# Kernel tuning notes

Measured on AMD Instinct MI355X. Metric: run time of the kernel, lower is better.

Reference implementation:

```python
import jax, jax.numpy as jnp
import numpy as np
from jax import lax

B, T, S = 8, 4096, 64  # batch, time steps, hidden states


def setup_inputs() -> dict:
    key = jax.random.key(0)
    k1, k2 = jax.random.split(key)
    # log-domain pairwise factors: log_factors[b, t, i, j] = log p(z_{t+1}=j, x_t | z_t=i)
    log_factors = jax.random.normal(k1, (B, T, S, S), dtype=jnp.float32)
    # initial log factor over the first state
    log_init = jax.random.normal(k2, (B, S), dtype=jnp.float32)
    return {"log_factors": log_factors, "log_init": log_init}


def reference(log_factors, log_init):
    """HMM forward algorithm: sequential logaddexp/add chain reduction over time.

    Equivalent to sequential_sum_product(logaddexp, add, log_factors, 'time')
    followed by adding log_init over 'state' and reducing all with logaddexp.
    Implemented as the O(T*S^2) alpha-recursion (vector carry) rather than the
    O(T*S^3) matrix chain -- same math, efficient form.
    """
    fs = jnp.moveaxis(log_factors, 1, 0)  # [T, B, S, S]

    def step(alpha, f_t):
        # alpha: [B, S] over state i ; f_t: [B, S, S] over (i, j)
        alpha_next = jax.nn.logsumexp(alpha[:, :, None] + f_t, axis=1)  # [B, S]
        return alpha_next, None

    alpha_T, _ = lax.scan(step, log_init, fs)
    return jax.nn.logsumexp(alpha_T, axis=-1)  # [B] log-normalizer
```

## Files before the change

### kernel.cpp

```cpp
#include <hip/hip_runtime.h>


#define HMM_B 8
#define HMM_T 4096
#define HMM_S 64
#define HMM_C 128
#define HMM_L (HMM_T / HMM_C)

typedef __attribute__((ext_vector_type(8))) short s16x8;
typedef __attribute__((ext_vector_type(4))) float f32x4;
typedef __attribute__((ext_vector_type(4))) unsigned int u32x4;

__device__ inline void gld16(const float* g, const float* l) {
  __builtin_amdgcn_global_load_lds((const __attribute__((address_space(1))) void*)g,
                                   (__attribute__((address_space(3))) void*)l, 16, 0, 0);
}

__device__ inline unsigned cvtpk(float lo, float hi) {
  unsigned r;
  asm("v_cvt_pk_bf16_f32 %0, %1, %2" : "=v"(r) : "v"(lo), "v"(hi));
  return r;
}

__device__ inline float dpp_fmax16(float x) {
  int xi = __float_as_int(x);
  x = fmaxf(x, __int_as_float(__builtin_amdgcn_mov_dpp(xi, 0xB1, 0xF, 0xF, 1)));
  xi = __float_as_int(x);
  x = fmaxf(x, __int_as_float(__builtin_amdgcn_mov_dpp(xi, 0x4E, 0xF, 0xF, 1)));
  xi = __float_as_int(x);
  x = fmaxf(x, __int_as_float(__builtin_amdgcn_mov_dpp(xi, 0x141, 0xF, 0xF, 1)));
  xi = __float_as_int(x);
  x = fmaxf(x, __int_as_float(__builtin_amdgcn_mov_dpp(xi, 0x140, 0xF, 0xF, 1)));
  return x;
}

__device__ inline float bflo(unsigned w) { return __uint_as_float(w << 16); }
__device__ inline float bfhi(unsigned w) { return __uint_as_float(w & 0xffff0000u); }


__global__ __launch_bounds__(256, 3)
void hmm_phase1(const float* __restrict__ lf, unsigned short* __restrict__ wsE,
                unsigned short* __restrict__ wsEt, float* __restrict__ wsM) {
  __shared__ struct {
    float fbuf[2][4096];
    unsigned short fB[4096];
    unsigned short escr[4][1408];
  } sm;

  const int tid = threadIdx.x;
  const int w   = tid >> 6;
  const int l   = tid & 63;
  const int wg  = blockIdx.x;
  const int bb  = wg >> 7;
  const int cc  = wg & (HMM_C - 1);
  const float* fbase = lf + ((size_t)(bb * HMM_T + cc * HMM_L)) * (HMM_S * HMM_S);

  auto issue = [&](int t) {
    const int par = t & 1;
    const float* fb = fbase + (size_t)t * 4096;
#pragma unroll
    for (int u = 0; u < 4; ++u) {
      int slot = (w * 4 + u) * 64 + l;
      int k    = slot >> 4;
      int q16  = slot & 15;
      const float* src = fb + k * 64 + ((q16 ^ (k & 7)) << 2);
      gld16(src, &sm.fbuf[par][(w * 4 + u) * 256]);
    }
  };

  issue(0);

  float mracc0 = 0.f, mracc1 = 0.f, mracc2 = 0.f, mracc3 = 0.f;
  const int c4 = l & 15, q = l >> 4;

  for (int t = 0; t < HMM_L; ++t) {
    const int par = t & 1;
    if (t + 1 < HMM_L) issue(t + 1);

    if (t < HMM_L - 1) asm volatile("s_waitcnt vmcnt(4)" ::: "memory");
    else               asm volatile("s_waitcnt vmcnt(0)" ::: "memory");
    __builtin_amdgcn_sched_barrier(0);

#pragma unroll
    for (int u = 0; u < 2; ++u) {
      const int g = 2 * w + (l >> 5);
      const int j = (l & 31) + 32 * u;
      float v[8];
#pragma unroll
      for (int e = 0; e < 8; ++e) {
        int k = 8 * g + e;
        v[e] = sm.fbuf[par][k * 64 + (((j >> 2) ^ (k & 7)) << 2) + (j & 3)];
      }
      unsigned p0 = cvtpk(__expf(v[0]), __expf(v[1]));
      unsigned p1 = cvtpk(__expf(v[2]), __expf(v[3]));
      unsigned p2 = cvtpk(__expf(v[4]), __expf(v[5]));
      unsigned p3 = cvtpk(__expf(v[6]), __expf(v[7]));
      int slot = ((g >> 2) * 4 + (j >> 4)) * 64 + ((g & 3) << 4) + (j & 15);
      u32x4 o; o.x = p0; o.y = p1; o.z = p2; o.w = p3;
      *(u32x4*)&sm.fB[slot * 8] = o;
    }

    asm volatile("s_waitcnt lgkmcnt(0)" ::: "memory");
    __builtin_amdgcn_sched_barrier(0);
    __builtin_amdgcn_s_barrier();

    s16x8 a0, a1;
    if (t == 0) {
      const int iloc = 16 * w + (l & 15);
      const int kb0 = (l >> 4) * 8, kb1 = 32 + (l >> 4) * 8;
#pragma unroll
      for (int e = 0; e < 8; ++e) {
        a0[e] = (short)((kb0 + e == iloc) ? 0x3F80 : 0);
        a1[e] = (short)((kb1 + e == iloc) ? 0x3F80 : 0);
      }
    } else {
      a0 = *(const s16x8*)&sm.escr[w][(l & 15) * 88 + ((l >> 4) * 8)];
      a1 = *(const s16x8*)&sm.escr[w][(l & 15) * 88 + 32 + ((l >> 4) * 8)];
    }

    f32x4 acc[4];
#pragma unroll
    for (int n = 0; n < 4; ++n) {
      s16x8 b0 = *(const s16x8*)&sm.fB[((0 + n) * 64 + l) * 8];
      s16x8 b1 = *(const s16x8*)&sm.fB[((4 + n) * 64 + l) * 8];
      f32x4 c = {0.f, 0.f, 0.f, 0.f};
      c = __builtin_amdgcn_mfma_f32_16x16x32_bf16(a0, b0, c, 0, 0, 0);
      c = __builtin_amdgcn_mfma_f32_16x16x32_bf16(a1, b1, c, 0, 0, 0);
      acc[n] = c;
    }

    float inv[4];
    {
      float m0 = fmaxf(fmaxf(acc[0][0], acc[1][0]), fmaxf(acc[2][0], acc[3][0]));
      float m1 = fmaxf(fmaxf(acc[0][1], acc[1][1]), fmaxf(acc[2][1], acc[3][1]));
      float m2 = fmaxf(fmaxf(acc[0][2], acc[1][2]), fmaxf(acc[2][2], acc[3][2]));
      float m3 = fmaxf(fmaxf(acc[0][3], acc[1][3]), fmaxf(acc[2][3], acc[3][3]));
      m0 = dpp_fmax16(m0); m1 = dpp_fmax16(m1);
      m2 = dpp_fmax16(m2); m3 = dpp_fmax16(m3);
      mracc0 += __log2f(m0); mracc1 += __log2f(m1);
      mracc2 += __log2f(m2); mracc3 += __log2f(m3);
      inv[0] = __builtin_amdgcn_rcpf(m0); inv[1] = __builtin_amdgcn_rcpf(m1);
      inv[2] = __builtin_amdgcn_rcpf(m2); inv[3] = __builtin_amdgcn_rcpf(m3);
    }
#pragma unroll
    for (int n = 0; n < 4; ++n) {
      unsigned p0 = cvtpk(acc[n][0] * inv[0], acc[n][1] * inv[1]);
      unsigned p1 = cvtpk(acc[n][2] * inv[2], acc[n][3] * inv[3]);
      sm.escr[w][(4 * q + 0) * 88 + 16 * n + c4] = (unsigned short)(p0 & 0xffffu);
      sm.escr[w][(4 * q + 1) * 88 + 16 * n + c4] = (unsigned short)(p0 >> 16);
      sm.escr[w][(4 * q + 2) * 88 + 16 * n + c4] = (unsigned short)(p1 & 0xffffu);
      sm.escr[w][(4 * q + 3) * 88 + 16 * n + c4] = (unsigned short)(p1 >> 16);
    }
    __syncthreads();
  }

  {
    const size_t cb = ((size_t)(bb * HMM_C + cc)) * 4096;
    const int j = tid & 63, p4 = tid >> 6;
    unsigned short o0[8], o1[8];
#pragma unroll
    for (int rl = 0; rl < 8; ++rl)  o0[rl] = sm.escr[p4][rl * 88 + j];
#pragma unroll
    for (int rl = 0; rl < 8; ++rl)  o1[rl] = sm.escr[p4][(rl + 8) * 88 + j];
    *(u32x4*)&wsEt[cb + j * 64 + p4 * 16]     = *(u32x4*)o0;
    *(u32x4*)&wsEt[cb + j * 64 + p4 * 16 + 8] = *(u32x4*)o1;

    const int r = tid >> 2, jq = tid & 3;
    u32x4 v0 = *(const u32x4*)&sm.escr[r >> 4][(r & 15) * 88 + jq * 16];
    u32x4 v1 = *(const u32x4*)&sm.escr[r >> 4][(r & 15) * 88 + jq * 16 + 8];
    *(u32x4*)&wsE[cb + r * 64 + jq * 16]     = v0;
    *(u32x4*)&wsE[cb + r * 64 + jq * 16 + 8] = v1;

    if (c4 == 0) {
      const float ln2 = 0.6931471805599453f;
      float* dst = wsM + (size_t)(bb * HMM_C + cc) * 64 + 16 * w + 4 * q;
      dst[0] = mracc0 * ln2; dst[1] = mracc1 * ln2;
      dst[2] = mracc2 * ln2; dst[3] = mracc3 * ln2;
    }
  }
}


__global__ __launch_bounds__(64)
void hmm_combine(const unsigned short* __restrict__ inE,
                 const unsigned short* __restrict__ inEt,
                 const float* __restrict__ inM, int inBS,
                 unsigned short* __restrict__ outE,
                 unsigned short* __restrict__ outEt,
                 float* __restrict__ outM, int outBS, int nOut) {
  __shared__ float sS[64];
  __shared__ float sM1[64];
  const int l = threadIdx.x, c4 = l & 15, q = l >> 4;
  const int b = blockIdx.x / nOut, p = blockIdx.x % nOut;
  const size_t li = (size_t)(b * inBS + 2 * p) * 4096;
  const size_t ri = li + 4096;
  const float* m1p = inM + (size_t)(b * inBS + 2 * p) * 64;

  float m2v = m1p[64 + l];
  float m1v = m1p[l];
  float mu = m2v;
  mu = fmaxf(mu, __shfl_xor(mu, 1));  mu = fmaxf(mu, __shfl_xor(mu, 2));
  mu = fmaxf(mu, __shfl_xor(mu, 4));  mu = fmaxf(mu, __shfl_xor(mu, 8));
  mu = fmaxf(mu, __shfl_xor(mu, 16)); mu = fmaxf(mu, __shfl_xor(mu, 32));
  sS[l] = __expf(m2v - mu);
  sM1[l] = m1v;
  __syncthreads();

  const unsigned short* E1 = inE + li;
  s16x8 afr[4][2];
#pragma unroll
  for (int m = 0; m < 4; ++m)
#pragma unroll
    for (int h = 0; h < 2; ++h)
      afr[m][h] = *(const s16x8*)&E1[(m * 16 + c4) * 64 + h * 32 + q * 8];

  const unsigned short* Et2 = inEt + ri;
  s16x8 bfr[2][4];
#pragma unroll
  for (int h = 0; h < 2; ++h) {
    f32x4 s0 = *(const f32x4*)&sS[h * 32 + q * 8];
    f32x4 s1 = *(const f32x4*)&sS[h * 32 + q * 8 + 4];
#pragma unroll
    for (int n = 0; n < 4; ++n) {
      u32x4 raw = *(const u32x4*)&Et2[(n * 16 + c4) * 64 + h * 32 + q * 8];
      unsigned p0 = cvtpk(bflo(raw.x) * s0[0], bfhi(raw.x) * s0[1]);
      unsigned p1 = cvtpk(bflo(raw.y) * s0[2], bfhi(raw.y) * s0[3]);
      unsigned p2 = cvtpk(bflo(raw.z) * s1[0], bfhi(raw.z) * s1[1]);
      unsigned p3 = cvtpk(bflo(raw.w) * s1[2], bfhi(raw.w) * s1[3]);
      u32x4 o; o.x = p0; o.y = p1; o.z = p2; o.w = p3;
      bfr[h][n] = *(s16x8*)&o;
    }
  }

  f32x4 acc[4][4];
#pragma unroll
  for (int m = 0; m < 4; ++m)
#pragma unroll
    for (int n = 0; n < 4; ++n) {
      f32x4 c = {0.f, 0.f, 0.f, 0.f};
      c = __builtin_amdgcn_mfma_f32_16x16x32_bf16(afr[m][0], bfr[0][n], c, 0, 0, 0);
      c = __builtin_amdgcn_mfma_f32_16x16x32_bf16(afr[m][1], bfr[1][n], c, 0, 0, 0);
      acc[m][n] = c;
    }

  const size_t oi = (size_t)(b * outBS + p) * 4096;
  unsigned short* Eo  = outE + oi;
  unsigned short* Eto = outEt + oi;
  float* mo = outM + (size_t)(b * outBS + p) * 64;

#pragma unroll
  for (int m = 0; m < 4; ++m) {
    float rmax[4];
#pragma unroll
    for (int r = 0; r < 4; ++r) {
      float v = fmaxf(fmaxf(acc[m][0][r], acc[m][1][r]),
                      fmaxf(acc[m][2][r], acc[m][3][r]));
      v = fmaxf(v, __shfl_xor(v, 1));
      v = fmaxf(v, __shfl_xor(v, 2));
      v = fmaxf(v, __shfl_xor(v, 4));
      v = fmaxf(v, __shfl_xor(v, 8));
      rmax[r] = v;
    }
    float inv[4] = {__builtin_amdgcn_rcpf(rmax[0]), __builtin_amdgcn_rcpf(rmax[1]),
                    __builtin_amdgcn_rcpf(rmax[2]), __builtin_amdgcn_rcpf(rmax[3])};
#pragma unroll
    for (int n = 0; n < 4; ++n) {
      unsigned p01 = cvtpk(acc[m][n][0] * inv[0], acc[m][n][1] * inv[1]);
      unsigned p23 = cvtpk(acc[m][n][2] * inv[2], acc[m][n][3] * inv[3]);
      unsigned long long packed = (unsigned long long)p01 |
                                  ((unsigned long long)p23 << 32);
      *(unsigned long long*)&Eto[(16 * n + c4) * 64 + 16 * m + 4 * q] = packed;
      Eo[(16 * m + 4 * q + 0) * 64 + 16 * n + c4] = (unsigned short)(p01 & 0xffffu);
      Eo[(16 * m + 4 * q + 1) * 64 + 16 * n + c4] = (unsigned short)(p01 >> 16);
      Eo[(16 * m + 4 * q + 2) * 64 + 16 * n + c4] = (unsigned short)(p23 & 0xffffu);
      Eo[(16 * m + 4 * q + 3) * 64 + 16 * n + c4] = (unsigned short)(p23 >> 16);
    }
    if (c4 == 0) {
#pragma unroll
      for (int r = 0; r < 4; ++r) {
        int i = 16 * m + 4 * q + r;
        mo[i] = sM1[i] + mu + __logf(rmax[r]);
      }
    }
  }
}


__global__ __launch_bounds__(64)
void hmm_final(const unsigned short* __restrict__ E, const float* __restrict__ M,
               int bs, const float* __restrict__ linit, float* __restrict__ out) {
  const int b = blockIdx.x, l = threadIdx.x;
  const unsigned short* Eb = E + (size_t)b * bs * 4096;
  float av = linit[b * 64 + l] + M[(size_t)b * bs * 64 + l];
  float mx = av;
  mx = fmaxf(mx, __shfl_xor(mx, 1));  mx = fmaxf(mx, __shfl_xor(mx, 2));
  mx = fmaxf(mx, __shfl_xor(mx, 4));  mx = fmaxf(mx, __shfl_xor(mx, 8));
  mx = fmaxf(mx, __shfl_xor(mx, 16)); mx = fmaxf(mx, __shfl_xor(mx, 32));
  float u = __expf(av - mx);
  float rs = 0.f;
#pragma unroll
  for (int e = 0; e < 8; ++e) {
    u32x4 raw = *(const u32x4*)&Eb[l * 64 + e * 8];
    rs += bflo(raw.x) + bfhi(raw.x) + bflo(raw.y) + bfhi(raw.y) +
          bflo(raw.z) + bfhi(raw.z) + bflo(raw.w) + bfhi(raw.w);
  }
  float s = u * rs;
  s += __shfl_xor(s, 1);  s += __shfl_xor(s, 2);  s += __shfl_xor(s, 4);
  s += __shfl_xor(s, 8);  s += __shfl_xor(s, 16); s += __shfl_xor(s, 32);
  if (l == 0) out[b] = mx + __logf(s);
}

extern "C" void kernel_launch(void* const* d_in, const int* in_sizes, int n_in,
                              void* d_out, int out_size, void* d_ws, size_t ws_size,
                              hipStream_t stream) {
  (void)in_sizes; (void)n_in; (void)out_size; (void)ws_size;
  const float* lf    = (const float*)d_in[0];
  const float* linit = (const float*)d_in[1];
  float* out = (float*)d_out;

  unsigned short* E_A  = (unsigned short*)d_ws;
  unsigned short* Et_A = E_A + (size_t)1024 * 4096;
  float*          M_A  = (float*)(Et_A + (size_t)1024 * 4096);
  unsigned short* E_B  = (unsigned short*)(M_A + (size_t)1024 * 64);
  unsigned short* Et_B = E_B + (size_t)512 * 4096;
  float*          M_B  = (float*)(Et_B + (size_t)512 * 4096);

  hmm_phase1<<<dim3(HMM_B * HMM_C), dim3(256), 0, stream>>>(lf, E_A, Et_A, M_A);

  hmm_combine<<<dim3(8 * 64), dim3(64), 0, stream>>>(E_A, Et_A, M_A, 128,
                                                     E_B, Et_B, M_B, 64, 64);
  hmm_combine<<<dim3(8 * 32), dim3(64), 0, stream>>>(E_B, Et_B, M_B, 64,
                                                     E_A, Et_A, M_A, 128, 32);
  hmm_combine<<<dim3(8 * 16), dim3(64), 0, stream>>>(E_A, Et_A, M_A, 128,
                                                     E_B, Et_B, M_B, 64, 16);
  hmm_combine<<<dim3(8 * 8),  dim3(64), 0, stream>>>(E_B, Et_B, M_B, 64,
                                                     E_A, Et_A, M_A, 128, 8);
  hmm_combine<<<dim3(8 * 4),  dim3(64), 0, stream>>>(E_A, Et_A, M_A, 128,
                                                     E_B, Et_B, M_B, 64, 4);
  hmm_combine<<<dim3(8 * 2),  dim3(64), 0, stream>>>(E_B, Et_B, M_B, 64,
                                                     E_A, Et_A, M_A, 128, 2);
  hmm_combine<<<dim3(8 * 1),  dim3(64), 0, stream>>>(E_A, Et_A, M_A, 128,
                                                     E_B, Et_B, M_B, 64, 1);

  hmm_final<<<dim3(HMM_B), dim3(64), 0, stream>>>(E_B, M_B, 64, linit, out);
}
```

Baseline: 208.2 us.

## Replace tree of combine launches with sequential 16-chunk combine and vector final pass

Result: slower. 229.2 us (+10.1%).

```diff
diff --git a/kernel.cpp b/kernel.cpp
--- a/kernel.cpp
+++ b/kernel.cpp
@@ -69,13 +69,13 @@
   };
 
   issue(0);
+  issue(1);
 
   float mracc0 = 0.f, mracc1 = 0.f, mracc2 = 0.f, mracc3 = 0.f;
   const int c4 = l & 15, q = l >> 4;
 
   for (int t = 0; t < HMM_L; ++t) {
     const int par = t & 1;
-    if (t + 1 < HMM_L) issue(t + 1);
 
     if (t < HMM_L - 1) asm volatile("s_waitcnt vmcnt(4)" ::: "memory");
     else               asm volatile("s_waitcnt vmcnt(0)" ::: "memory");
@@ -103,6 +103,9 @@
     asm volatile("s_waitcnt lgkmcnt(0)" ::: "memory");
     __builtin_amdgcn_sched_barrier(0);
     __builtin_amdgcn_s_barrier();
+    __builtin_amdgcn_sched_barrier(0);
+
+    if (t + 2 < HMM_L) issue(t + 2);
 
     s16x8 a0, a1;
     if (t == 0) {
@@ -151,8 +154,14 @@
       sm.escr[w][(4 * q + 2) * 88 + 16 * n + c4] = (unsigned short)(p1 & 0xffffu);
       sm.escr[w][(4 * q + 3) * 88 + 16 * n + c4] = (unsigned short)(p1 >> 16);
     }
-    __syncthreads();
-  }
+
+    asm volatile("s_waitcnt lgkmcnt(0)" ::: "memory");
+    __builtin_amdgcn_sched_barrier(0);
+    __builtin_amdgcn_s_barrier();
+    __builtin_amdgcn_sched_barrier(0);
+  }
+
+  __syncthreads();
 
   {
     const size_t cb = ((size_t)(bb * HMM_C + cc)) * 4096;
@@ -165,11 +174,13 @@
     *(u32x4*)&wsEt[cb + j * 64 + p4 * 16]     = *(u32x4*)o0;
     *(u32x4*)&wsEt[cb + j * 64 + p4 * 16 + 8] = *(u32x4*)o1;
 
-    const int r = tid >> 2, jq = tid & 3;
-    u32x4 v0 = *(const u32x4*)&sm.escr[r >> 4][(r & 15) * 88 + jq * 16];
-    u32x4 v1 = *(const u32x4*)&sm.escr[r >> 4][(r & 15) * 88 + jq * 16 + 8];
-    *(u32x4*)&wsE[cb + r * 64 + jq * 16]     = v0;
-    *(u32x4*)&wsE[cb + r * 64 + jq * 16 + 8] = v1;
+    if ((cc & 15) == 0) {
+      const int r = tid >> 2, jq = tid & 3;
+      u32x4 v0 = *(const u32x4*)&sm.escr[r >> 4][(r & 15) * 88 + jq * 16];
+      u32x4 v1 = *(const u32x4*)&sm.escr[r >> 4][(r & 15) * 88 + jq * 16 + 8];
+      *(u32x4*)&wsE[cb + r * 64 + jq * 16]     = v0;
+      *(u32x4*)&wsE[cb + r * 64 + jq * 16 + 8] = v1;
+    }
 
     if (c4 == 0) {
       const float ln2 = 0.6931471805599453f;
@@ -182,129 +193,215 @@
 
 
 __global__ __launch_bounds__(64)
-void hmm_combine(const unsigned short* __restrict__ inE,
-                 const unsigned short* __restrict__ inEt,
-                 const float* __restrict__ inM, int inBS,
-                 unsigned short* __restrict__ outE,
-                 unsigned short* __restrict__ outEt,
-                 float* __restrict__ outM, int outBS, int nOut) {
+void hmm_combine16(const unsigned short* __restrict__ inE,
+                   const unsigned short* __restrict__ inEt,
+                   const float* __restrict__ inM,
+                   unsigned short* __restrict__ outEt,
+                   float* __restrict__ outM) {
   __shared__ float sS[64];
-  __shared__ float sM1[64];
+  __shared__ float sM[64];
+  __shared__ unsigned short pL[4096];
+
   const int l = threadIdx.x, c4 = l & 15, q = l >> 4;
-  const int b = blockIdx.x / nOut, p = blockIdx.x % nOut;
-  const size_t li = (size_t)(b * inBS + 2 * p) * 4096;
-  const size_t ri = li + 4096;
-  const float* m1p = inM + (size_t)(b * inBS + 2 * p) * 64;
-
-  float m2v = m1p[64 + l];
-  float m1v = m1p[l];
-  float mu = m2v;
-  mu = fmaxf(mu, __shfl_xor(mu, 1));  mu = fmaxf(mu, __shfl_xor(mu, 2));
-  mu = fmaxf(mu, __shfl_xor(mu, 4));  mu = fmaxf(mu, __shfl_xor(mu, 8));
-  mu = fmaxf(mu, __shfl_xor(mu, 16)); mu = fmaxf(mu, __shfl_xor(mu, 32));
-  sS[l] = __expf(m2v - mu);
-  sM1[l] = m1v;
-  __syncthreads();
-
-  const unsigned short* E1 = inE + li;
+  const int b = blockIdx.x >> 3, g = blockIdx.x & 7;
+  const int cbase = b * HMM_C + g * 16;
+
   s16x8 afr[4][2];
 #pragma unroll
   for (int m = 0; m < 4; ++m)
 #pragma unroll
     for (int h = 0; h < 2; ++h)
-      afr[m][h] = *(const s16x8*)&E1[(m * 16 + c4) * 64 + h * 32 + q * 8];
-
-  const unsigned short* Et2 = inEt + ri;
-  s16x8 bfr[2][4];
-#pragma unroll
-  for (int h = 0; h < 2; ++h) {
-    f32x4 s0 = *(const f32x4*)&sS[h * 32 + q * 8];
-    f32x4 s1 = *(const f32x4*)&sS[h * 32 + q * 8 + 4];
-#pragma unroll
-    for (int n = 0; n < 4; ++n) {
-      u32x4 raw = *(const u32x4*)&Et2[(n * 16 + c4) * 64 + h * 32 + q * 8];
-      unsigned p0 = cvtpk(bflo(raw.x) * s0[0], bfhi(raw.x) * s0[1]);
-      unsigned p1 = cvtpk(bflo(raw.y) * s0[2], bfhi(raw.y) * s0[3]);
-      unsigned p2 = cvtpk(bflo(raw.z) * s1[0], bfhi(raw.z) * s1[1]);
-      unsigned p3 = cvtpk(bflo(raw.w) * s1[2], bfhi(raw.w) * s1[3]);
-      u32x4 o; o.x = p0; o.y = p1; o.z = p2; o.w = p3;
-      bfr[h][n] = *(s16x8*)&o;
-    }
-  }
-
-  f32x4 acc[4][4];
-#pragma unroll
-  for (int m = 0; m < 4; ++m)
-#pragma unroll
-    for (int n = 0; n < 4; ++n) {
-      f32x4 c = {0.f, 0.f, 0.f, 0.f};
-      c = __builtin_amdgcn_mfma_f32_16x16x32_bf16(afr[m][0], bfr[0][n], c, 0, 0, 0);
-      c = __builtin_amdgcn_mfma_f32_16x16x32_bf16(afr[m][1], bfr[1][n], c, 0, 0, 0);
-      acc[m][n] = c;
-    }
-
-  const size_t oi = (size_t)(b * outBS + p) * 4096;
-  unsigned short* Eo  = outE + oi;
-  unsigned short* Eto = outEt + oi;
-  float* mo = outM + (size_t)(b * outBS + p) * 64;
-
-#pragma unroll
-  for (int m = 0; m < 4; ++m) {
-    float rmax[4];
-#pragma unroll
-    for (int r = 0; r < 4; ++r) {
-      float v = fmaxf(fmaxf(acc[m][0][r], acc[m][1][r]),
-                      fmaxf(acc[m][2][r], acc[m][3][r]));
-      v = fmaxf(v, __shfl_xor(v, 1));
-      v = fmaxf(v, __shfl_xor(v, 2));
-      v = fmaxf(v, __shfl_xor(v, 4));
-      v = fmaxf(v, __shfl_xor(v, 8));
-      rmax[r] = v;
-    }
-    float inv[4] = {__builtin_amdgcn_rcpf(rmax[0]), __builtin_amdgcn_rcpf(rmax[1]),
-                    __builtin_amdgcn_rcpf(rmax[2]), __builtin_amdgcn_rcpf(rmax[3])};
-#pragma unroll
-    for (int n = 0; n < 4; ++n) {
-      unsigned p01 = cvtpk(acc[m][n][0] * inv[0], acc[m][n][1] * inv[1]);
-      unsigned p23 = cvtpk(acc[m][n][2] * inv[2], acc[m][n][3] * inv[3]);
-      unsigned long long packed = (unsigned long long)p01 |
-                                  ((unsigned long long)p23 << 32);
-      *(unsigned long long*)&Eto[(16 * n + c4) * 64 + 16 * m + 4 * q] = packed;
-      Eo[(16 * m + 4 * q + 0) * 64 + 16 * n + c4] = (unsigned short)(p01 & 0xffffu);
-      Eo[(16 * m + 4 * q + 1) * 64 + 16 * n + c4] = (unsigned short)(p01 >> 16);
-      Eo[(16 * m + 4 * q + 2) * 64 + 16 * n + c4] = (unsigned short)(p23 & 0xffffu);
-      Eo[(16 * m + 4 * q + 3) * 64 + 16 * n + c4] = (unsigned short)(p23 >> 16);
-    }
+      afr[m][h] = *(const s16x8*)&inE[(size_t)cbase * 4096 +
+                                      (m * 16 + c4) * 64 + h * 32 + q * 8];
+  sM[l] = inM[(size_t)cbase * 64 + l];
+
+  u32x4 braw[2][4];
+  float mv;
+  {
+    const unsigned short* Et = inEt + (size_t)(cbase + 1) * 4096;
+#pragma unroll
+    for (int h = 0; h < 2; ++h)
+#pragma unroll
+      for (int n = 0; n < 4; ++n)
+        braw[h][n] = *(const u32x4*)&Et[(n * 16 + c4) * 64 + h * 32 + q * 8];
+    mv = inM[(size_t)(cbase + 1) * 64 + l];
+  }
+
+  for (int c = 1; c < 16; ++c) {
+    u32x4 bcur[2][4];
+#pragma unroll
+    for (int h = 0; h < 2; ++h)
+#pragma unroll
+      for (int n = 0; n < 4; ++n) bcur[h][n] = braw[h][n];
+    float mcur = mv;
+    if (c < 15) {
+      const unsigned short* Et = inEt + (size_t)(cbase + c + 1) * 4096;
+#pragma unroll
+      for (int h = 0; h < 2; ++h)
+#pragma unroll
+        for (int n = 0; n < 4; ++n)
+          braw[h][n] = *(const u32x4*)&Et[(n * 16 + c4) * 64 + h * 32 + q * 8];
+      mv = inM[(size_t)(cbase + c + 1) * 64 + l];
+    }
+
+    float nu = mcur;
+    nu = fmaxf(nu, __shfl_xor(nu, 1));  nu = fmaxf(nu, __shfl_xor(nu, 2));
+    nu = fmaxf(nu, __shfl_xor(nu, 4));  nu = fmaxf(nu, __shfl_xor(nu, 8));
+    nu = fmaxf(nu, __shfl_xor(nu, 16)); nu = fmaxf(nu, __shfl_xor(nu, 32));
+    sS[l] = __expf(mcur - nu);
+
+    s16x8 bfr[2][4];
+#pragma unroll
+    for (int h = 0; h < 2; ++h) {
+      f32x4 s0 = *(const f32x4*)&sS[h * 32 + q * 8];
+      f32x4 s1 = *(const f32x4*)&sS[h * 32 + q * 8 + 4];
+#pragma unroll
+      for (int n = 0; n < 4; ++n) {
+        u32x4 raw = bcur[h][n];
+        unsigned p0 = cvtpk(bflo(raw.x) * s0[0], bfhi(raw.x) * s0[1]);
+        unsigned p1 = cvtpk(bflo(raw.y) * s0[2], bfhi(raw.y) * s0[3]);
+        unsigned p2 = cvtpk(bflo(raw.z) * s1[0], bfhi(raw.z) * s1[1]);
+        unsigned p3 = cvtpk(bflo(raw.w) * s1[2], bfhi(raw.w) * s1[3]);
+        u32x4 o; o.x = p0; o.y = p1; o.z = p2; o.w = p3;
+        bfr[h][n] = *(s16x8*)&o;
+      }
+    }
+
+    f32x4 acc[4][4];
+#pragma unroll
+    for (int m = 0; m < 4; ++m)
+#pragma unroll
+      for (int n = 0; n < 4; ++n) {
+        f32x4 cc2 = {0.f, 0.f, 0.f, 0.f};
+        cc2 = __builtin_amdgcn_mfma_f32_16x16x32_bf16(afr[m][0], bfr[0][n], cc2, 0, 0, 0);
+        cc2 = __builtin_amdgcn_mfma_f32_16x16x32_bf16(afr[m][1], bfr[1][n], cc2, 0, 0, 0);
+        acc[m][n] = cc2;
+      }
+
+    float rmax[4][4];
+#pragma unroll
+    for (int m = 0; m < 4; ++m)
+#pragma unroll
+      for (int r = 0; r < 4; ++r) {
+        float v = fmaxf(fmaxf(acc[m][0][r], acc[m][1][r]),
+                        fmaxf(acc[m][2][r], acc[m][3][r]));
+        v = fmaxf(v, __shfl_xor(v, 1));
+        v = fmaxf(v, __shfl_xor(v, 2));
+        v = fmaxf(v, __shfl_xor(v, 4));
+        v = fmaxf(v, __shfl_xor(v, 8));
+        rmax[m][r] = v;
+      }
     if (c4 == 0) {
 #pragma unroll
-      for (int r = 0; r < 4; ++r) {
-        int i = 16 * m + 4 * q + r;
-        mo[i] = sM1[i] + mu + __logf(rmax[r]);
-      }
-    }
-  }
-}
-
+      for (int m = 0; m < 4; ++m)
+#pragma unroll
+        for (int r = 0; r < 4; ++r)
+          sM[16 * m + 4 * q + r] += nu + __logf(rmax[m][r]);
+    }
+
+    if (c < 15) {
+#pragma unroll
+      for (int m = 0; m < 4; ++m) {
+        float i0 = __builtin_amdgcn_rcpf(rmax[m][0]);
+        float i1 = __builtin_amdgcn_rcpf(rmax[m][1]);
+        float i2 = __builtin_amdgcn_rcpf(rmax[m][2]);
+        float i3 = __builtin_amdgcn_rcpf(rmax[m][3]);
+#pragma unroll
+        for (int n = 0; n < 4; ++n) {
+          unsigned p01 = cvtpk(acc[m][n][0] * i0, acc[m][n][1] * i1);
+          unsigned p23 = cvtpk(acc[m][n][2] * i2, acc[m][n][3] * i3);
+          pL[(16 * m + 4 * q + 0) * 64 + 16 * n + c4] = (unsigned short)(p01 & 0xffffu);
+          pL[(16 * m + 4 * q + 1) * 64 + 16 * n + c4] = (unsigned short)(p01 >> 16);
+          pL[(16 * m + 4 * q + 2) * 64 + 16 * n + c4] = (unsigned short)(p23 & 0xffffu);
+          pL[(16 * m + 4 * q + 3) * 64 + 16 * n + c4] = (unsigned short)(p23 >> 16);
+        }
+      }
+#pragma unroll
+      for (int m = 0; m < 4; ++m)
+#pragma unroll
+        for (int h = 0; h < 2; ++h)
+          afr[m][h] = *(const s16x8*)&pL[(m * 16 + c4) * 64 + h * 32 + q * 8];
+    } else {
+      const size_t oi = (size_t)(b * 8 + g) * 4096;
+#pragma unroll
+      for (int m = 0; m < 4; ++m) {
+        float i0 = __builtin_amdgcn_rcpf(rmax[m][0]);
+        float i1 = __builtin_amdgcn_rcpf(rmax[m][1]);
+        float i2 = __builtin_amdgcn_rcpf(rmax[m][2]);
+        float i3 = __builtin_amdgcn_rcpf(rmax[m][3]);
+#pragma unroll
+        for (int n = 0; n < 4; ++n) {
+          unsigned p01 = cvtpk(acc[m][n][0] * i0, acc[m][n][1] * i1);
+          unsigned p23 = cvtpk(acc[m][n][2] * i2, acc[m][n][3] * i3);
+          unsigned long long packed = (unsigned long long)p01 |
+                                      ((unsigned long long)p23 << 32);
+          *(unsigned long long*)&outEt[oi + (16 * n + c4) * 64 + 16 * m + 4 * q] = packed;
+        }
+      }
+      outM[(size_t)(b * 8 + g) * 64 + l] = sM[l];
+    }
+  }
+}
+
+
+__device__ inline float rdlane(float v, int t) {
+  return __int_as_float(__builtin_amdgcn_readlane(__float_as_int(v), t));
+}
 
 __global__ __launch_bounds__(64)
-void hmm_final(const unsigned short* __restrict__ E, const float* __restrict__ M,
-               int bs, const float* __restrict__ linit, float* __restrict__ out) {
+void hmm_final(const unsigned short* __restrict__ Et, const float* __restrict__ M,
+               const float* __restrict__ linit, float* __restrict__ out) {
   const int b = blockIdx.x, l = threadIdx.x;
-  const unsigned short* Eb = E + (size_t)b * bs * 4096;
-  float av = linit[b * 64 + l] + M[(size_t)b * bs * 64 + l];
-  float mx = av;
+  float alpha = linit[b * 64 + l];
+
+  int4 e[8]; float mg;
+  {
+    const int4* src = (const int4*)(Et + (size_t)(b * 8) * 4096 + (size_t)l * 64);
+#pragma unroll
+    for (int u = 0; u < 8; ++u) e[u] = src[u];
+    mg = M[(size_t)(b * 8) * 64 + l];
+  }
+
+  for (int g = 0; g < 8; ++g) {
+    int4 ec[8];
+#pragma unroll
+    for (int u = 0; u < 8; ++u) ec[u] = e[u];
+    float mcur = mg;
+    if (g < 7) {
+      const int4* src = (const int4*)(Et + (size_t)(b * 8 + g + 1) * 4096 + (size_t)l * 64);
+#pragma unroll
+      for (int u = 0; u < 8; ++u) e[u] = src[u];
+      mg = M[(size_t)(b * 8 + g + 1) * 64 + l];
+    }
+
+    float av = alpha + mcur;
+    float mx = av;
+    mx = fmaxf(mx, __shfl_xor(mx, 1));  mx = fmaxf(mx, __shfl_xor(mx, 2));
+    mx = fmaxf(mx, __shfl_xor(mx, 4));  mx = fmaxf(mx, __shfl_xor(mx, 8));
+    mx = fmaxf(mx, __shfl_xor(mx, 16)); mx = fmaxf(mx, __shfl_xor(mx, 32));
+    float wv = __expf(av - mx);
+    float s = 0.f;
+#pragma unroll
+    for (int u = 0; u < 8; ++u) {
+      unsigned w0 = (unsigned)ec[u].x, w1 = (unsigned)ec[u].y;
+      unsigned w2 = (unsigned)ec[u].z, w3 = (unsigned)ec[u].w;
+      s = fmaf(rdlane(wv, 8 * u + 0), bflo(w0), s);
+      s = fmaf(rdlane(wv, 8 * u + 1), bfhi(w0), s);
+      s = fmaf(rdlane(wv, 8 * u + 2), bflo(w1), s);
+      s = fmaf(rdlane(wv, 8 * u + 3), bfhi(w1), s);
+      s = fmaf(rdlane(wv, 8 * u + 4), bflo(w2), s);
+      s = fmaf(rdlane(wv, 8 * u + 5), bfhi(w2), s);
+      s = fmaf(rdlane(wv, 8 * u + 6), bflo(w3), s);
+      s = fmaf(rdlane(wv, 8 * u + 7), bfhi(w3), s);
+    }
+    alpha = mx + __logf(s);
+  }
+
+  float mx = alpha;
   mx = fmaxf(mx, __shfl_xor(mx, 1));  mx = fmaxf(mx, __shfl_xor(mx, 2));
   mx = fmaxf(mx, __shfl_xor(mx, 4));  mx = fmaxf(mx, __shfl_xor(mx, 8));
   mx = fmaxf(mx, __shfl_xor(mx, 16)); mx = fmaxf(mx, __shfl_xor(mx, 32));
-  float u = __expf(av - mx);
-  float rs = 0.f;
-#pragma unroll
-  for (int e = 0; e < 8; ++e) {
-    u32x4 raw = *(const u32x4*)&Eb[l * 64 + e * 8];
-    rs += bflo(raw.x) + bfhi(raw.x) + bflo(raw.y) + bfhi(raw.y) +
-          bflo(raw.z) + bfhi(raw.z) + bflo(raw.w) + bfhi(raw.w);
-  }
-  float s = u * rs;
+  float s = __expf(alpha - mx);
   s += __shfl_xor(s, 1);  s += __shfl_xor(s, 2);  s += __shfl_xor(s, 4);
   s += __shfl_xor(s, 8);  s += __shfl_xor(s, 16); s += __shfl_xor(s, 32);
   if (l == 0) out[b] = mx + __logf(s);
@@ -321,26 +418,10 @@
   unsigned short* E_A  = (unsigned short*)d_ws;
   unsigned short* Et_A = E_A + (size_t)1024 * 4096;
   float*          M_A  = (float*)(Et_A + (size_t)1024 * 4096);
-  unsigned short* E_B  = (unsigned short*)(M_A + (size_t)1024 * 64);
-  unsigned short* Et_B = E_B + (size_t)512 * 4096;
-  float*          M_B  = (float*)(Et_B + (size_t)512 * 4096);
+  unsigned short* Et_B = (unsigned short*)(M_A + (size_t)1024 * 64);
+  float*          M_B  = (float*)(Et_B + (size_t)64 * 4096);
 
   hmm_phase1<<<dim3(HMM_B * HMM_C), dim3(256), 0, stream>>>(lf, E_A, Et_A, M_A);
-
-  hmm_combine<<<dim3(8 * 64), dim3(64), 0, stream>>>(E_A, Et_A, M_A, 128,
-                                                     E_B, Et_B, M_B, 64, 64);
-  hmm_combine<<<dim3(8 * 32), dim3(64), 0, stream>>>(E_B, Et_B, M_B, 64,
-                                                     E_A, Et_A, M_A, 128, 32);
-  hmm_combine<<<dim3(8 * 16), dim3(64), 0, stream>>>(E_A, Et_A, M_A, 128,
-                                                     E_B, Et_B, M_B, 64, 16);
-  hmm_combine<<<dim3(8 * 8),  dim3(64), 0, stream>>>(E_B, Et_B, M_B, 64,
-                                                     E_A, Et_A, M_A, 128, 8);
-  hmm_combine<<<dim3(8 * 4),  dim3(64), 0, stream>>>(E_A, Et_A, M_A, 128,
-                                                     E_B, Et_B, M_B, 64, 4);
-  hmm_combine<<<dim3(8 * 2),  dim3(64), 0, stream>>>(E_B, Et_B, M_B, 64,
-                                                     E_A, Et_A, M_A, 128, 2);
-  hmm_combine<<<dim3(8 * 1),  dim3(64), 0, stream>>>(E_A, Et_A, M_A, 128,
-                                                     E_B, Et_B, M_B, 64, 1);
-
-  hmm_final<<<dim3(HMM_B), dim3(64), 0, stream>>>(E_B, M_B, 64, linit, out);
-}
+  hmm_combine16<<<dim3(64), dim3(64), 0, stream>>>(E_A, Et_A, M_A, Et_B, M_B);
+  hmm_final<<<dim3(HMM_B), dim3(64), 0, stream>>>(Et_B, M_B, linit, out);
+}
```
